# Optimization experiments

Measured on AMD Instinct MI355X. Metric: run time of the kernel, lower is better.

## Reference

```python
import jax, jax.numpy as jnp
import numpy as np

IN_CH, OUT_CH, IN_W, K, PAD = 64, 64, 2048, 3, 1
OUT_W = IN_W + 2 * PAD - K + 1  # 2048


def setup_inputs() -> dict:
    key = jax.random.key(0)
    k1, k2, k3 = jax.random.split(key, 3)
    x = jax.random.normal(k1, (32, IN_CH, IN_W), dtype=jnp.float32)
    weights = jax.random.normal(k2, (OUT_W, OUT_CH, IN_CH, K), dtype=jnp.float32)
    bias = jax.random.normal(k3, (OUT_CH, OUT_W), dtype=jnp.float32)
    return {"x": x, "weights": weights, "bias": bias}


def reference(x, weights, bias):
    # x: (B, IC, W); weights: (OW, OC, IC, K); bias: (OC, OW)
    xp = jnp.pad(x, ((0, 0), (0, 0), (PAD, PAD)))  # (B, IC, W+2p)
    # Gather sliding windows: patches[b, ic, w, k] = xp[b, ic, w + k]
    idx = jnp.arange(OUT_W)[:, None] + jnp.arange(K)[None, :]  # (OW, K)
    patches = xp[:, :, idx]  # (B, IC, OW, K)
    # Per-position unshared contraction over (ic, k)
    out = jnp.einsum('bcwk,wock->bow', patches, weights)  # (B, OC, OW)
    return out + bias[None, :, :]
```

## Files before the change

kernel.cpp:

```cpp
#include <hip/hip_runtime.h>
#include <hip/hip_bf16.h>

typedef _Float16 f16x4 __attribute__((ext_vector_type(4)));
typedef _Float16 f16x8 __attribute__((ext_vector_type(8)));
typedef float f32x4 __attribute__((ext_vector_type(4)));

#define IN_CH   64
#define OUT_CH  64
#define W_TOT   2048
#define KW      3
#define B_TOT   32
#define CK      192
#define LDSTRIDE 200

__global__ __launch_bounds__(256, 4)
void lc1d_kernel(const float* __restrict__ x,
                 const float* __restrict__ wts,
                 const float* __restrict__ bias,
                 float* __restrict__ out) {
    __shared__ _Float16 Wt[OUT_CH * LDSTRIDE];
    __shared__ _Float16 Xp[B_TOT * LDSTRIDE];

    const int tid = threadIdx.x;
    const int bid = blockIdx.x;
    const int w = (bid & 7) * 256 + (bid >> 3);

    const float* wsrc = wts + (size_t)w * (OUT_CH * CK);
    #pragma unroll
    for (int i = 0; i < 12; ++i) {
        int e = i * 1024 + tid * 4;
        float4 v = *reinterpret_cast<const float4*>(wsrc + e);
        int r = e / CK;
        int c = e - r * CK;
        f16x4 h = { (_Float16)v.x, (_Float16)v.y, (_Float16)v.z, (_Float16)v.w };
        *reinterpret_cast<f16x4*>(&Wt[r * LDSTRIDE + c]) = h;
    }

    #pragma unroll
    for (int j = 0; j < 8; ++j) {
        int p = tid + 256 * j;
        int b = p >> 6;
        int c = p & 63;
        const float* row = x + (size_t)p * W_TOT;
        #pragma unroll
        for (int k = 0; k < KW; ++k) {
            int v = w - 1 + k;
            float xv = (v >= 0 && v < W_TOT) ? row[v] : 0.0f;
            Xp[b * LDSTRIDE + c * 3 + k] = (_Float16)xv;
        }
    }

    __syncthreads();

    const int lane = tid & 63;
    const int wv   = tid >> 6;
    const int l15  = lane & 15;
    const int kg   = lane >> 4;

    const _Float16* Xb = &Xp[l15 * LDSTRIDE + kg * 8];
    const _Float16* Wb = &Wt[(wv * 16 + l15) * LDSTRIDE + kg * 8];

    f32x4 acc0 = {0.f, 0.f, 0.f, 0.f};
    f32x4 acc1 = {0.f, 0.f, 0.f, 0.f};
    #pragma unroll
    for (int kk = 0; kk < 6; ++kk) {
        f16x8 a0 = *reinterpret_cast<const f16x8*>(Xb + kk * 32);
        f16x8 a1 = *reinterpret_cast<const f16x8*>(Xb + 16 * LDSTRIDE + kk * 32);
        f16x8 bf = *reinterpret_cast<const f16x8*>(Wb + kk * 32);
        acc0 = __builtin_amdgcn_mfma_f32_16x16x32_f16(a0, bf, acc0, 0, 0, 0);
        acc1 = __builtin_amdgcn_mfma_f32_16x16x32_f16(a1, bf, acc1, 0, 0, 0);
    }

    const int o = wv * 16 + l15;
    const float bv = bias[o * W_TOT + w];
    #pragma unroll
    for (int r = 0; r < 4; ++r) {
        int b0 = kg * 4 + r;
        out[((size_t)(b0 * OUT_CH + o)) * W_TOT + w] = acc0[r] + bv;
        int b1 = 16 + kg * 4 + r;
        out[((size_t)(b1 * OUT_CH + o)) * W_TOT + w] = acc1[r] + bv;
    }
}

extern "C" void kernel_launch(void* const* d_in, const int* in_sizes, int n_in,
                              void* d_out, int out_size, void* d_ws, size_t ws_size,
                              hipStream_t stream) {
    const float* x    = (const float*)d_in[0];
    const float* wts  = (const float*)d_in[1];
    const float* bias = (const float*)d_in[2];
    float* out = (float*)d_out;
    hipLaunchKernelGGL(lc1d_kernel, dim3(2048), dim3(256), 0, stream,
                       x, wts, bias, out);
}
```

Measured before the change: 219.3 us.

## Split into patch-build prepass and double-buffered async-LDS main kernel

Adds a prepass kernel that builds fp16 im2col patches for every output position in a workspace laid out contiguously per position. The main kernel now processes 8 positions and half the output channels per block. It streams fp32 weights and patches into LDS through global_load_lds into a double buffer, with an XOR swizzle, and converts weights to fp16 in registers. It also writes 4 consecutive positions per vector store. The aim is to replace the strided per-element gather of x and the synchronous weight staging with coalesced async loads overlapped with MFMA, at the cost of an extra launch and a workspace round trip.

```diff
diff --git a/kernel.cpp b/kernel.cpp
--- a/kernel.cpp
+++ b/kernel.cpp
@@ -1,84 +1,168 @@
 #include <hip/hip_runtime.h>
-#include <hip/hip_bf16.h>
+#include <stdint.h>
 
-typedef _Float16 f16x4 __attribute__((ext_vector_type(4)));
 typedef _Float16 f16x8 __attribute__((ext_vector_type(8)));
 typedef float f32x4 __attribute__((ext_vector_type(4)));
 
-#define IN_CH   64
-#define OUT_CH  64
-#define W_TOT   2048
-#define KW      3
-#define B_TOT   32
-#define CK      192
-#define LDSTRIDE 200
+#define W_TOT 2048
+#define CK    192
 
-__global__ __launch_bounds__(256, 4)
-void lc1d_kernel(const float* __restrict__ x,
-                 const float* __restrict__ wts,
-                 const float* __restrict__ bias,
-                 float* __restrict__ out) {
-    __shared__ _Float16 Wt[OUT_CH * LDSTRIDE];
-    __shared__ _Float16 Xp[B_TOT * LDSTRIDE];
+static __device__ __forceinline__ f16x8 cvt8(f32x4 a, f32x4 b) {
+    f16x8 r;
+    r[0] = (_Float16)a[0]; r[1] = (_Float16)a[1]; r[2] = (_Float16)a[2]; r[3] = (_Float16)a[3];
+    r[4] = (_Float16)b[0]; r[5] = (_Float16)b[1]; r[6] = (_Float16)b[2]; r[7] = (_Float16)b[3];
+    return r;
+}
+
+__global__ __launch_bounds__(256, 2)
+void xp_build(const float* __restrict__ x, _Float16* __restrict__ xP) {
+    __shared__ _Float16 Xt[144 * 72];
+    const int tid = threadIdx.x;
+    const int b   = blockIdx.x >> 4;
+    const int wt  = (blockIdx.x & 15) << 7;
+
+    {
+        const int c = tid & 63, q = tid >> 6;
+        const float* xr = x + ((size_t)(b * 64 + c)) * W_TOT;
+        #pragma unroll
+        for (int k = 0; k < 9; ++k) {
+            int iw = q * 36 + k * 4;
+            int wg = wt - 4 + iw;
+            float v0, v1, v2, v3;
+            if (wg >= 0 && wg + 3 < W_TOT) {
+                float4 v = *(const float4*)(xr + wg);
+                v0 = v.x; v1 = v.y; v2 = v.z; v3 = v.w;
+            } else {
+                v0 = (wg + 0 >= 0 && wg + 0 < W_TOT) ? xr[wg + 0] : 0.f;
+                v1 = (wg + 1 >= 0 && wg + 1 < W_TOT) ? xr[wg + 1] : 0.f;
+                v2 = (wg + 2 >= 0 && wg + 2 < W_TOT) ? xr[wg + 2] : 0.f;
+                v3 = (wg + 3 >= 0 && wg + 3 < W_TOT) ? xr[wg + 3] : 0.f;
+            }
+            Xt[(iw + 0) * 72 + c] = (_Float16)v0;
+            Xt[(iw + 1) * 72 + c] = (_Float16)v1;
+            Xt[(iw + 2) * 72 + c] = (_Float16)v2;
+            Xt[(iw + 3) * 72 + c] = (_Float16)v3;
+        }
+    }
+    __syncthreads();
+    {
+        const int wp = tid >> 1, h = tid & 1;
+        _Float16* ob = xP + (size_t)(wt + wp) * 6144 + b * 192 + h * 96;
+        #pragma unroll
+        for (int cg = 0; cg < 4; ++cg) {
+            int c0 = h * 32 + cg * 8;
+            f16x8 r0 = *(const f16x8*)&Xt[(wp + 3) * 72 + c0];
+            f16x8 r1 = *(const f16x8*)&Xt[(wp + 4) * 72 + c0];
+            f16x8 r2 = *(const f16x8*)&Xt[(wp + 5) * 72 + c0];
+            _Float16 t[24];
+            #pragma unroll
+            for (int m = 0; m < 8; ++m) { t[m*3] = r0[m]; t[m*3+1] = r1[m]; t[m*3+2] = r2[m]; }
+            f16x8 o0, o1, o2;
+            #pragma unroll
+            for (int m = 0; m < 8; ++m) { o0[m] = t[m]; o1[m] = t[8+m]; o2[m] = t[16+m]; }
+            *(f16x8*)(ob + cg * 24 + 0)  = o0;
+            *(f16x8*)(ob + cg * 24 + 8)  = o1;
+            *(f16x8*)(ob + cg * 24 + 16) = o2;
+        }
+    }
+}
+
+static __device__ __forceinline__ void stage_w(const char* wsrc, char* ldsw,
+                                               const char* xsrc, char* ldsx,
+                                               int wv, int lane) {
+    #pragma unroll
+    for (int i = 0; i < 6; ++i) {
+        int d = wv * 6144 + i * 1024 + lane * 16;
+        int r = d / 768;
+        __builtin_amdgcn_global_load_lds(
+            (const __attribute__((address_space(1))) uint32_t*)(wsrc + (d ^ ((r & 7) << 4))),
+            (__attribute__((address_space(3))) uint32_t*)(ldsw + d), 16, 0, 0);
+    }
+    #pragma unroll
+    for (int i = 0; i < 3; ++i) {
+        int d = wv * 3072 + i * 1024 + lane * 16;
+        int r = d / 384;
+        __builtin_amdgcn_global_load_lds(
+            (const __attribute__((address_space(1))) uint32_t*)(xsrc + (d ^ ((r & 7) << 4))),
+            (__attribute__((address_space(3))) uint32_t*)(ldsx + d), 16, 0, 0);
+    }
+}
+
+static __device__ __forceinline__ void compute_w(const char* wrow, const char* xrow,
+                                                 int kg, int sm, int smx, f32x4& acc) {
+    #pragma unroll
+    for (int ks = 0; ks < 6; ++ks) {
+        f32x4 b0 = *(const f32x4*)(wrow + (((ks * 128 + kg * 32) + 0)  ^ sm));
+        f32x4 b1 = *(const f32x4*)(wrow + (((ks * 128 + kg * 32) + 16) ^ sm));
+        f16x8 bw = cvt8(b0, b1);
+        f16x8 a  = *(const f16x8*)(xrow + ((ks * 64 + kg * 16) ^ smx));
+        acc = __builtin_amdgcn_mfma_f32_16x16x32_f16(a, bw, acc, 0, 0, 0);
+    }
+}
+
+__global__ __launch_bounds__(256, 2)
+void lc1d_main(const _Float16* __restrict__ xP,
+               const float* __restrict__ wts,
+               const float* __restrict__ bias,
+               float* __restrict__ out) {
+    __shared__ char WfL[2][24576];
+    __shared__ char XpL[2][12288];
 
     const int tid = threadIdx.x;
     const int bid = blockIdx.x;
-    const int w = (bid & 7) * 256 + (bid >> 3);
+    const int xcd = bid & 7, idx = bid >> 3;
+    const int wc  = xcd * 32 + (idx >> 1);
+    const int bo  = idx & 1;
+    const int w0  = wc * 8;
 
-    const float* wsrc = wts + (size_t)w * (OUT_CH * CK);
-    #pragma unroll
-    for (int i = 0; i < 12; ++i) {
-        int e = i * 1024 + tid * 4;
-        float4 v = *reinterpret_cast<const float4*>(wsrc + e);
-        int r = e / CK;
-        int c = e - r * CK;
-        f16x4 h = { (_Float16)v.x, (_Float16)v.y, (_Float16)v.z, (_Float16)v.w };
-        *reinterpret_cast<f16x4*>(&Wt[r * LDSTRIDE + c]) = h;
-    }
+    const int lane = tid & 63, wv = tid >> 6;
+    const int bt = wv >> 1, ot = wv & 1;
+    const int l15 = lane & 15, kg = lane >> 4;
+    const int o_loc = ot * 16 + l15;
+    const int o = bo * 32 + o_loc;
+    const int sm  = (o_loc & 7) << 4;
+    const int smx = (l15 & 7) << 4;
 
-    #pragma unroll
-    for (int j = 0; j < 8; ++j) {
-        int p = tid + 256 * j;
-        int b = p >> 6;
-        int c = p & 63;
-        const float* row = x + (size_t)p * W_TOT;
-        #pragma unroll
-        for (int k = 0; k < KW; ++k) {
-            int v = w - 1 + k;
-            float xv = (v >= 0 && v < W_TOT) ? row[v] : 0.0f;
-            Xp[b * LDSTRIDE + c * 3 + k] = (_Float16)xv;
-        }
-    }
+    const char* wgbase = (const char*)wts + (size_t)w0 * 49152 + (size_t)bo * 24576;
+    const char* xgbase = (const char*)xP + (size_t)w0 * 12288;
+    const char* wrow = &WfL[0][0] + o_loc * 768;
+    const char* xrow = &XpL[0][0] + (bt * 16 + l15) * 384;
+    const int BUF1W = 24576, BUF1X = 12288;
 
+    stage_w(wgbase, &WfL[0][0], xgbase, &XpL[0][0], wv, lane);
+    const f32x4 bg0 = *(const f32x4*)(bias + (size_t)o * W_TOT + w0);
+    const f32x4 bg1 = *(const f32x4*)(bias + (size_t)o * W_TOT + w0 + 4);
     __syncthreads();
 
-    const int lane = tid & 63;
-    const int wv   = tid >> 6;
-    const int l15  = lane & 15;
-    const int kg   = lane >> 4;
+    f32x4 a0 = {0.f,0.f,0.f,0.f}, a1 = a0, a2 = a0, a3 = a0;
 
-    const _Float16* Xb = &Xp[l15 * LDSTRIDE + kg * 8];
-    const _Float16* Wb = &Wt[(wv * 16 + l15) * LDSTRIDE + kg * 8];
-
-    f32x4 acc0 = {0.f, 0.f, 0.f, 0.f};
-    f32x4 acc1 = {0.f, 0.f, 0.f, 0.f};
-    #pragma unroll
-    for (int kk = 0; kk < 6; ++kk) {
-        f16x8 a0 = *reinterpret_cast<const f16x8*>(Xb + kk * 32);
-        f16x8 a1 = *reinterpret_cast<const f16x8*>(Xb + 16 * LDSTRIDE + kk * 32);
-        f16x8 bf = *reinterpret_cast<const f16x8*>(Wb + kk * 32);
-        acc0 = __builtin_amdgcn_mfma_f32_16x16x32_f16(a0, bf, acc0, 0, 0, 0);
-        acc1 = __builtin_amdgcn_mfma_f32_16x16x32_f16(a1, bf, acc1, 0, 0, 0);
-    }
-
-    const int o = wv * 16 + l15;
-    const float bv = bias[o * W_TOT + w];
+    stage_w(wgbase + 1*49152, &WfL[0][0]+BUF1W, xgbase + 1*12288, &XpL[0][0]+BUF1X, wv, lane);
+    compute_w(wrow,          xrow,          kg, sm, smx, a0);  __syncthreads();
+    stage_w(wgbase + 2*49152, &WfL[0][0],   xgbase + 2*12288, &XpL[0][0],          wv, lane);
+    compute_w(wrow + BUF1W,  xrow + BUF1X,  kg, sm, smx, a1);  __syncthreads();
+    stage_w(wgbase + 3*49152, &WfL[0][0]+BUF1W, xgbase + 3*12288, &XpL[0][0]+BUF1X, wv, lane);
+    compute_w(wrow,          xrow,          kg, sm, smx, a2);  __syncthreads();
+    stage_w(wgbase + 4*49152, &WfL[0][0],   xgbase + 4*12288, &XpL[0][0],          wv, lane);
+    compute_w(wrow + BUF1W,  xrow + BUF1X,  kg, sm, smx, a3);
     #pragma unroll
     for (int r = 0; r < 4; ++r) {
-        int b0 = kg * 4 + r;
-        out[((size_t)(b0 * OUT_CH + o)) * W_TOT + w] = acc0[r] + bv;
-        int b1 = 16 + kg * 4 + r;
-        out[((size_t)(b1 * OUT_CH + o)) * W_TOT + w] = acc1[r] + bv;
+        f32x4 v = { a0[r] + bg0[0], a1[r] + bg0[1], a2[r] + bg0[2], a3[r] + bg0[3] };
+        *(f32x4*)(out + ((size_t)((bt * 16 + kg * 4 + r) * 64 + o)) * W_TOT + w0) = v;
+    }
+    __syncthreads();
+
+    a0 = {0.f,0.f,0.f,0.f}; a1 = a0; a2 = a0; a3 = a0;
+    stage_w(wgbase + 5*49152, &WfL[0][0]+BUF1W, xgbase + 5*12288, &XpL[0][0]+BUF1X, wv, lane);
+    compute_w(wrow,          xrow,          kg, sm, smx, a0);  __syncthreads();
+    stage_w(wgbase + 6*49152, &WfL[0][0],   xgbase + 6*12288, &XpL[0][0],          wv, lane);
+    compute_w(wrow + BUF1W,  xrow + BUF1X,  kg, sm, smx, a1);  __syncthreads();
+    stage_w(wgbase + 7*49152, &WfL[0][0]+BUF1W, xgbase + 7*12288, &XpL[0][0]+BUF1X, wv, lane);
+    compute_w(wrow,          xrow,          kg, sm, smx, a2);  __syncthreads();
+    compute_w(wrow + BUF1W,  xrow + BUF1X,  kg, sm, smx, a3);
+    #pragma unroll
+    for (int r = 0; r < 4; ++r) {
+        f32x4 v = { a0[r] + bg1[0], a1[r] + bg1[1], a2[r] + bg1[2], a3[r] + bg1[3] };
+        *(f32x4*)(out + ((size_t)((bt * 16 + kg * 4 + r) * 64 + o)) * W_TOT + w0 + 4) = v;
     }
 }
 
@@ -89,6 +173,7 @@
     const float* wts  = (const float*)d_in[1];
     const float* bias = (const float*)d_in[2];
     float* out = (float*)d_out;
-    hipLaunchKernelGGL(lc1d_kernel, dim3(2048), dim3(256), 0, stream,
-                       x, wts, bias, out);
+    _Float16* xP = (_Float16*)d_ws;
+    hipLaunchKernelGGL(xp_build, dim3(512), dim3(256), 0, stream, x, xP);
+    hipLaunchKernelGGL(lc1d_main, dim3(512), dim3(256), 0, stream, xP, wts, bias, out);
 }
```

New measurement: 192.8 us. -12.1%, faster.
